# Kernel tuning notes

Hardware: AMD Instinct MI355X
Metric: run time of the kernel (lower is better)

## Reference

```python
import jax, jax.numpy as jnp
import numpy as np

E, N, D, H = 16, 2048, 1024, 4096  # experts, tokens/expert, dim, hidden

def setup_inputs() -> dict:
    key = jax.random.key(0)
    k1, k2, k3 = jax.random.split(key, 3)
    std1 = 1.0 / np.sqrt(H)  # init_ uses last dim of w1 -> hidden_dim
    std2 = 1.0 / np.sqrt(D)  # last dim of w2 -> dim
    x = jax.random.normal(k1, (E, N, D), dtype=jnp.float32)
    w1 = jax.random.uniform(k2, (E, D, H), dtype=jnp.float32, minval=-std1, maxval=std1)
    w2 = jax.random.uniform(k3, (E, H, D), dtype=jnp.float32, minval=-std2, maxval=std2)
    b1 = jnp.zeros((H,), dtype=jnp.float32)
    b2 = jnp.zeros((D,), dtype=jnp.float32)
    return {"x": x, "w1": w1, "w2": w2, "b1": b1, "b2": b2}

def reference(x, w1, w2, b1, b2):
    # grouped two-layer FFN per expert; dropout p=0 is identity
    hidden = jnp.einsum('end,edh->enh', x, w1) + b1
    hidden = jax.nn.gelu(hidden, approximate=False)  # nn.GELU (exact erf)
    out = jnp.einsum('enh,ehd->end', hidden, w2) + b2
    return out
```

## Files before the change

kernel.cpp:

```cpp
#include <hip/hip_runtime.h>
#include <cstdint>
#include <cstddef>

#define NE 16
#define NTOK 2048
#define DDIM 1024
#define HDIM 4096

typedef unsigned short u16;
typedef __bf16 bf16x8 __attribute__((ext_vector_type(8)));
typedef float f32x4 __attribute__((ext_vector_type(4)));

typedef __attribute__((address_space(1))) const void as1_cvoid;
typedef __attribute__((address_space(3))) void as3_void;

__device__ __forceinline__ void load_lds16(const void* g, void* l) {
    __builtin_amdgcn_global_load_lds((as1_cvoid*)g, (as3_void*)l, 16, 0, 0);
}

__device__ __forceinline__ u16 f2bf(float f) {
    uint32_t x = __float_as_uint(f);
    x += 0x7FFFu + ((x >> 16) & 1u);
    return (u16)(x >> 16);
}

__global__ void cvt_x_kernel(const float* __restrict__ in, u16* __restrict__ out, size_t n4) {
    size_t i = (size_t)blockIdx.x * blockDim.x + threadIdx.x;
    if (i >= n4) return;
    float4 v = ((const float4*)in)[i];
    uint32_t lo = (uint32_t)f2bf(v.x) | ((uint32_t)f2bf(v.y) << 16);
    uint32_t hi = (uint32_t)f2bf(v.z) | ((uint32_t)f2bf(v.w) << 16);
    ((uint2*)out)[i] = make_uint2(lo, hi);
}

__global__ void transpose_cvt_kernel(const float* __restrict__ in, u16* __restrict__ out,
                                     int R, int C) {
    __shared__ u16 tile[32][33];
    int e = blockIdx.z;
    const float* pin = in + (size_t)e * R * C;
    u16* pout = out + (size_t)e * R * C;
    int c0 = blockIdx.x * 32, r0 = blockIdx.y * 32;
#pragma unroll
    for (int i = 0; i < 4; ++i) {
        int r = r0 + threadIdx.y + i * 8;
        tile[threadIdx.y + i * 8][threadIdx.x] = f2bf(pin[(size_t)r * C + c0 + threadIdx.x]);
    }
    __syncthreads();
#pragma unroll
    for (int i = 0; i < 4; ++i) {
        int c = c0 + threadIdx.y + i * 8;
        pout[(size_t)c * R + r0 + threadIdx.x] = tile[threadIdx.x][threadIdx.y + i * 8];
    }
}

template <bool GELU_BF16>
__global__ void __launch_bounds__(256)
gemm_bt_kernel(const u16* __restrict__ A, const u16* __restrict__ Bt,
               const float* __restrict__ bias, void* __restrict__ Cout,
               int M, int K, int Nout) {
    __shared__ u16 As[128 * 64];
    __shared__ u16 Bs[128 * 64];

    const int e = blockIdx.z;
    const u16* Ae = A + (size_t)e * M * K;
    const u16* Be = Bt + (size_t)e * Nout * K;

    const int t = threadIdx.x;
    const int wave = t >> 6;
    const int lane = t & 63;

    const int m_blk = blockIdx.y * 128;
    const int n_blk = blockIdx.x * 128;
    const int wm = (wave >> 1) * 64;
    const int wn = (wave & 1) * 64;

    const int ld_row = wave * 32 + (lane >> 3);
    const int ld_col = (lane & 7) * 8;
    const u16* a_g = Ae + (size_t)(m_blk + ld_row) * K + ld_col;
    const u16* b_g = Be + (size_t)(n_blk + ld_row) * K + ld_col;
    u16* a_l = As + wave * 4 * 512;
    u16* b_l = Bs + wave * 4 * 512;

    f32x4 acc[4][4];
#pragma unroll
    for (int i = 0; i < 4; ++i)
#pragma unroll
        for (int j = 0; j < 4; ++j)
            acc[i][j] = (f32x4){0.f, 0.f, 0.f, 0.f};

    const int frag_row_a = wm + (lane & 15);
    const int frag_row_b = wn + (lane & 15);
    const int frag_k = (lane >> 4) * 8;

    for (int k0 = 0; k0 < K; k0 += 64) {
        __syncthreads();
#pragma unroll
        for (int i = 0; i < 4; ++i) {
            load_lds16(a_g + (size_t)i * 8 * K + k0, a_l + i * 512);
            load_lds16(b_g + (size_t)i * 8 * K + k0, b_l + i * 512);
        }
        __syncthreads();
#pragma unroll
        for (int ks = 0; ks < 2; ++ks) {
            bf16x8 af[4], bf[4];
#pragma unroll
            for (int i = 0; i < 4; ++i)
                af[i] = *(const bf16x8*)&As[(frag_row_a + i * 16) * 64 + ks * 32 + frag_k];
#pragma unroll
            for (int j = 0; j < 4; ++j)
                bf[j] = *(const bf16x8*)&Bs[(frag_row_b + j * 16) * 64 + ks * 32 + frag_k];
#pragma unroll
            for (int i = 0; i < 4; ++i)
#pragma unroll
                for (int j = 0; j < 4; ++j)
                    acc[i][j] = __builtin_amdgcn_mfma_f32_16x16x32_bf16(af[i], bf[j], acc[i][j], 0, 0, 0);
        }
    }

    const int rbase = (lane >> 4) * 4;
    const int cbase = lane & 15;
#pragma unroll
    for (int i = 0; i < 4; ++i) {
#pragma unroll
        for (int j = 0; j < 4; ++j) {
            const int col = n_blk + wn + j * 16 + cbase;
            const float bv = bias[col];
#pragma unroll
            for (int r = 0; r < 4; ++r) {
                const int row = m_blk + wm + i * 16 + rbase + r;
                float v = acc[i][j][r] + bv;
                if (GELU_BF16) {
                    float g = 0.5f * v * (1.0f + erff(v * 0.70710678118654752f));
                    ((u16*)Cout)[(size_t)e * M * Nout + (size_t)row * Nout + col] = f2bf(g);
                } else {
                    ((float*)Cout)[(size_t)e * M * Nout + (size_t)row * Nout + col] = v;
                }
            }
        }
    }
}

extern "C" void kernel_launch(void* const* d_in, const int* in_sizes, int n_in,
                              void* d_out, int out_size, void* d_ws, size_t ws_size,
                              hipStream_t stream) {
    (void)in_sizes; (void)n_in; (void)out_size; (void)ws_size;
    const float* x  = (const float*)d_in[0];
    const float* w1 = (const float*)d_in[1];
    const float* w2 = (const float*)d_in[2];
    const float* b1 = (const float*)d_in[3];
    const float* b2 = (const float*)d_in[4];
    float* out = (float*)d_out;

    char* ws = (char*)d_ws;
    u16* xb  = (u16*)ws;
    u16* w1t = (u16*)(ws + (size_t)NE * NTOK * DDIM * 2);
    u16* w2t = (u16*)(ws + (size_t)NE * NTOK * DDIM * 2 + (size_t)NE * HDIM * DDIM * 2);
    u16* hid = (u16*)(ws + (size_t)NE * NTOK * DDIM * 2 + (size_t)2 * NE * HDIM * DDIM * 2);

    {
        size_t n4 = (size_t)NE * NTOK * DDIM / 4;
        cvt_x_kernel<<<(unsigned)((n4 + 255) / 256), 256, 0, stream>>>(x, xb, n4);
    }
    transpose_cvt_kernel<<<dim3(HDIM / 32, DDIM / 32, NE), dim3(32, 8), 0, stream>>>(w1, w1t, DDIM, HDIM);
    transpose_cvt_kernel<<<dim3(DDIM / 32, HDIM / 32, NE), dim3(32, 8), 0, stream>>>(w2, w2t, HDIM, DDIM);

    gemm_bt_kernel<true><<<dim3(HDIM / 128, NTOK / 128, NE), 256, 0, stream>>>(
        xb, w1t, b1, (void*)hid, NTOK, DDIM, HDIM);

    gemm_bt_kernel<false><<<dim3(DDIM / 128, NTOK / 128, NE), 256, 0, stream>>>(
        hid, w2t, b2, (void*)out, NTOK, HDIM, DDIM);
}
```

Before: 1.629 ms.

## Replace GEMM with 256x256 tile, 8-wave, double-buffered swizzled LDS pipeline

The simple 128x128 single-buffered GEMM is replaced by a 256x256 tile kernel with 8 waves per block. It uses 128KB of LDS split into double-buffered A/B halves with XOR-swizzled chunks to avoid bank conflicts. Loads for the next k-tile are interleaved with MFMA phases under explicit vmcnt/lgkmcnt waits, s_barrier, and setprio. The goal is higher data reuse per block and overlap of global loads with MFMA. In exchange it relies on hand-tuned inline asm waits whose correctness depends on exact load counts, and the larger LDS use likely limits occupancy despite the launch bound of 2.

```diff
diff --git a/kernel.cpp b/kernel.cpp
--- a/kernel.cpp
+++ b/kernel.cpp
@@ -10,6 +10,7 @@
 typedef unsigned short u16;
 typedef __bf16 bf16x8 __attribute__((ext_vector_type(8)));
 typedef float f32x4 __attribute__((ext_vector_type(4)));
+typedef unsigned int u32x4 __attribute__((ext_vector_type(4)));
 
 typedef __attribute__((address_space(1))) const void as1_cvoid;
 typedef __attribute__((address_space(3))) void as3_void;
@@ -22,6 +23,22 @@
     uint32_t x = __float_as_uint(f);
     x += 0x7FFFu + ((x >> 16) & 1u);
     return (u16)(x >> 16);
+}
+
+#define S_BARRIER() asm volatile("s_barrier" ::: "memory")
+#define WAIT_VM(N) asm volatile("s_waitcnt vmcnt(" #N ")" ::: "memory")
+#define WAIT_LGKM0()                                        \
+    do {                                                    \
+        asm volatile("s_waitcnt lgkmcnt(0)" ::: "memory");  \
+        __builtin_amdgcn_sched_barrier(0);                  \
+    } while (0)
+
+#define MFMA16(a, b, c) __builtin_amdgcn_mfma_f32_16x16x32_bf16((a), (b), (c), 0, 0, 0)
+
+__device__ __forceinline__ bf16x8 lds_read_b128(uint32_t byte_off) {
+    u32x4 r;
+    asm volatile("ds_read_b128 %0, %1" : "=v"(r) : "v"(byte_off));
+    return __builtin_bit_cast(bf16x8, r);
 }
 
 __global__ void cvt_x_kernel(const float* __restrict__ in, u16* __restrict__ out, size_t n4) {
@@ -53,87 +70,152 @@
     }
 }
 
-template <bool GELU_BF16>
-__global__ void __launch_bounds__(256)
-gemm_bt_kernel(const u16* __restrict__ A, const u16* __restrict__ Bt,
+template <bool GELU>
+__global__ void __launch_bounds__(512, 2)
+gemm256_kernel(const u16* __restrict__ A, const u16* __restrict__ Bt,
                const float* __restrict__ bias, void* __restrict__ Cout,
                int M, int K, int Nout) {
-    __shared__ u16 As[128 * 64];
-    __shared__ u16 Bs[128 * 64];
+    __shared__ u16 ldsU[65536];
 
     const int e = blockIdx.z;
     const u16* Ae = A + (size_t)e * M * K;
     const u16* Be = Bt + (size_t)e * Nout * K;
 
-    const int t = threadIdx.x;
-    const int wave = t >> 6;
-    const int lane = t & 63;
-
-    const int m_blk = blockIdx.y * 128;
-    const int n_blk = blockIdx.x * 128;
-    const int wm = (wave >> 1) * 64;
-    const int wn = (wave & 1) * 64;
-
-    const int ld_row = wave * 32 + (lane >> 3);
-    const int ld_col = (lane & 7) * 8;
-    const u16* a_g = Ae + (size_t)(m_blk + ld_row) * K + ld_col;
-    const u16* b_g = Be + (size_t)(n_blk + ld_row) * K + ld_col;
-    u16* a_l = As + wave * 4 * 512;
-    u16* b_l = Bs + wave * 4 * 512;
-
-    f32x4 acc[4][4];
-#pragma unroll
-    for (int i = 0; i < 4; ++i)
-#pragma unroll
-        for (int j = 0; j < 4; ++j)
-            acc[i][j] = (f32x4){0.f, 0.f, 0.f, 0.f};
-
-    const int frag_row_a = wm + (lane & 15);
-    const int frag_row_b = wn + (lane & 15);
-    const int frag_k = (lane >> 4) * 8;
-
-    for (int k0 = 0; k0 < K; k0 += 64) {
-        __syncthreads();
-#pragma unroll
-        for (int i = 0; i < 4; ++i) {
-            load_lds16(a_g + (size_t)i * 8 * K + k0, a_l + i * 512);
-            load_lds16(b_g + (size_t)i * 8 * K + k0, b_l + i * 512);
-        }
-        __syncthreads();
-#pragma unroll
-        for (int ks = 0; ks < 2; ++ks) {
-            bf16x8 af[4], bf[4];
-#pragma unroll
-            for (int i = 0; i < 4; ++i)
-                af[i] = *(const bf16x8*)&As[(frag_row_a + i * 16) * 64 + ks * 32 + frag_k];
-#pragma unroll
-            for (int j = 0; j < 4; ++j)
-                bf[j] = *(const bf16x8*)&Bs[(frag_row_b + j * 16) * 64 + ks * 32 + frag_k];
-#pragma unroll
-            for (int i = 0; i < 4; ++i)
-#pragma unroll
-                for (int j = 0; j < 4; ++j)
-                    acc[i][j] = __builtin_amdgcn_mfma_f32_16x16x32_bf16(af[i], bf[j], acc[i][j], 0, 0, 0);
-        }
-    }
-
-    const int rbase = (lane >> 4) * 4;
-    const int cbase = lane & 15;
-#pragma unroll
-    for (int i = 0; i < 4; ++i) {
+    const int tid = threadIdx.x;
+    const int wave = tid >> 6, lane = tid & 63;
+    const int wr = wave >> 2;
+    const int wc = wave & 3;
+
+    const int m_blk = blockIdx.y * 256, n_blk = blockIdx.x * 256;
+
+    const int schunk = (lane & 3) ^ ((lane >> 3) & 3);
+    const u16* aG = Ae + (size_t)(m_blk + wave * 32 + (lane >> 2)) * K + schunk * 8;
+    const u16* bG = Be + (size_t)(n_blk + wave * 32 + (lane >> 2)) * K + schunk * 8;
+    const size_t rowJ = (size_t)16 * K;
+
+    const int p = lane & 15, q = lane >> 4;
+    const int sq = q ^ ((p >> 1) & 3);
+    const uint32_t ardB = (uint32_t)((wr * 128 + p) * 64 + sq * 16);
+    const uint32_t brdB = (uint32_t)((wc * 64 + p) * 64 + sq * 16);
+
+    f32x4 acc[8][4];
+#pragma unroll
+    for (int i = 0; i < 8; ++i)
+#pragma unroll
+        for (int j = 0; j < 4; ++j) acc[i][j] = (f32x4){0.f, 0.f, 0.f, 0.f};
+
+    const int NT = K >> 6;
+
+    {
+        u16* dA0 = ldsU + wave * 1024;
+        u16* dA1 = ldsU + 8192 + wave * 1024;
+        u16* dB0 = ldsU + 32768 + wave * 1024;
+        u16* dB1 = ldsU + 40960 + wave * 1024;
+        load_lds16(aG, dA0);       load_lds16(aG + rowJ, dA0 + 512);
+        load_lds16(bG, dB0);       load_lds16(bG + rowJ, dB0 + 512);
+        load_lds16(aG + 32, dA1);  load_lds16(aG + 32 + rowJ, dA1 + 512);
+        load_lds16(bG + 32, dB1);  load_lds16(bG + 32 + rowJ, dB1 + 512);
+    }
+    WAIT_VM(4);
+    S_BARRIER();
+
+    for (int t = 0; t < NT; ++t) {
+        const bool hn = (t + 1 < NT);
+        const uint32_t buf = (uint32_t)(t & 1), nb = buf ^ 1u;
+        const uint32_t aP0 = (buf * 2 + 0) * 16384u;
+        const uint32_t aP1 = (buf * 2 + 1) * 16384u;
+        const uint32_t bP0 = 65536u + (buf * 2 + 0) * 16384u;
+        const uint32_t bP1 = 65536u + (buf * 2 + 1) * 16384u;
+        u16* nA0 = ldsU + (nb * 2 + 0) * 8192 + wave * 1024;
+        u16* nA1 = ldsU + (nb * 2 + 1) * 8192 + wave * 1024;
+        u16* nB0 = ldsU + 32768 + (nb * 2 + 0) * 8192 + wave * 1024;
+        u16* nB1 = ldsU + 32768 + (nb * 2 + 1) * 8192 + wave * 1024;
+        const u16* gA = aG + (size_t)(t + 1) * 64;
+        const u16* gB = bG + (size_t)(t + 1) * 64;
+
+        bf16x8 af[8], bf0, bf1;
+
+#pragma unroll
+        for (int i = 0; i < 8; ++i) af[i] = lds_read_b128(aP0 + ardB + (uint32_t)i * 1024u);
+        bf0 = lds_read_b128(bP0 + brdB);
+        bf1 = lds_read_b128(bP0 + brdB + 1024u);
+        if (hn) { load_lds16(gA, nA0); load_lds16(gA + rowJ, nA0 + 512); }
+        S_BARRIER();
+        WAIT_LGKM0();
+        __builtin_amdgcn_s_setprio(1);
+#pragma unroll
+        for (int i = 0; i < 8; ++i) {
+            acc[i][0] = MFMA16(af[i], bf0, acc[i][0]);
+            acc[i][1] = MFMA16(af[i], bf1, acc[i][1]);
+        }
+        __builtin_amdgcn_s_setprio(0);
+        S_BARRIER();
+
+        bf0 = lds_read_b128(bP0 + brdB + 2048u);
+        bf1 = lds_read_b128(bP0 + brdB + 3072u);
+        if (hn) { load_lds16(gB, nB0); load_lds16(gB + rowJ, nB0 + 512); }
+        S_BARRIER();
+        WAIT_LGKM0();
+        __builtin_amdgcn_s_setprio(1);
+#pragma unroll
+        for (int i = 0; i < 8; ++i) {
+            acc[i][2] = MFMA16(af[i], bf0, acc[i][2]);
+            acc[i][3] = MFMA16(af[i], bf1, acc[i][3]);
+        }
+        __builtin_amdgcn_s_setprio(0);
+        if (hn) { WAIT_VM(4); } else { WAIT_VM(0); }
+        S_BARRIER();
+
+#pragma unroll
+        for (int i = 0; i < 8; ++i) af[i] = lds_read_b128(aP1 + ardB + (uint32_t)i * 1024u);
+        bf0 = lds_read_b128(bP1 + brdB);
+        bf1 = lds_read_b128(bP1 + brdB + 1024u);
+        if (hn) { load_lds16(gA + 32, nA1); load_lds16(gA + 32 + rowJ, nA1 + 512); }
+        S_BARRIER();
+        WAIT_LGKM0();
+        __builtin_amdgcn_s_setprio(1);
+#pragma unroll
+        for (int i = 0; i < 8; ++i) {
+            acc[i][0] = MFMA16(af[i], bf0, acc[i][0]);
+            acc[i][1] = MFMA16(af[i], bf1, acc[i][1]);
+        }
+        __builtin_amdgcn_s_setprio(0);
+        S_BARRIER();
+
+        bf0 = lds_read_b128(bP1 + brdB + 2048u);
+        bf1 = lds_read_b128(bP1 + brdB + 3072u);
+        if (hn) { load_lds16(gB + 32, nB1); load_lds16(gB + 32 + rowJ, nB1 + 512); }
+        S_BARRIER();
+        WAIT_LGKM0();
+        __builtin_amdgcn_s_setprio(1);
+#pragma unroll
+        for (int i = 0; i < 8; ++i) {
+            acc[i][2] = MFMA16(af[i], bf0, acc[i][2]);
+            acc[i][3] = MFMA16(af[i], bf1, acc[i][3]);
+        }
+        __builtin_amdgcn_s_setprio(0);
+        if (hn) { WAIT_VM(4); }
+        S_BARRIER();
+    }
+
+    const int rb = (lane >> 4) * 4;
+    const int cb = lane & 15;
+    const size_t eoff = (size_t)e * M * Nout;
+#pragma unroll
+    for (int i = 0; i < 8; ++i) {
 #pragma unroll
         for (int j = 0; j < 4; ++j) {
-            const int col = n_blk + wn + j * 16 + cbase;
+            const int col = n_blk + wc * 64 + j * 16 + cb;
             const float bv = bias[col];
 #pragma unroll
             for (int r = 0; r < 4; ++r) {
-                const int row = m_blk + wm + i * 16 + rbase + r;
+                const int row = m_blk + wr * 128 + i * 16 + rb + r;
                 float v = acc[i][j][r] + bv;
-                if (GELU_BF16) {
+                if (GELU) {
                     float g = 0.5f * v * (1.0f + erff(v * 0.70710678118654752f));
-                    ((u16*)Cout)[(size_t)e * M * Nout + (size_t)row * Nout + col] = f2bf(g);
+                    ((u16*)Cout)[eoff + (size_t)row * Nout + col] = f2bf(g);
                 } else {
-                    ((float*)Cout)[(size_t)e * M * Nout + (size_t)row * Nout + col] = v;
+                    ((float*)Cout)[eoff + (size_t)row * Nout + col] = v;
                 }
             }
         }
@@ -164,9 +246,9 @@
     transpose_cvt_kernel<<<dim3(HDIM / 32, DDIM / 32, NE), dim3(32, 8), 0, stream>>>(w1, w1t, DDIM, HDIM);
     transpose_cvt_kernel<<<dim3(DDIM / 32, HDIM / 32, NE), dim3(32, 8), 0, stream>>>(w2, w2t, HDIM, DDIM);
 
-    gemm_bt_kernel<true><<<dim3(HDIM / 128, NTOK / 128, NE), 256, 0, stream>>>(
+    gemm256_kernel<true><<<dim3(HDIM / 256, NTOK / 256, NE), 512, 0, stream>>>(
         xb, w1t, b1, (void*)hid, NTOK, DDIM, HDIM);
 
-    gemm_bt_kernel<false><<<dim3(DDIM / 128, NTOK / 128, NE), 256, 0, stream>>>(
+    gemm256_kernel<false><<<dim3(DDIM / 256, NTOK / 256, NE), 512, 0, stream>>>(
         hid, w2t, b2, (void*)out, NTOK, HDIM, DDIM);
 }
```

After: 1.319 ms. -19.1%, faster.
